# Optimization experiments

Measured on AMD Instinct MI355X. Metric: run time of the kernel, lower is better.

Reference implementation:

```python
import jax, jax.numpy as jnp
import numpy as np

N = 16384
IN_DIM = 128
OUT_DIM = 128
NUM_TYPES = 8


def setup_inputs() -> dict:
    key = jax.random.key(0)
    k1, k2, k3, k4 = jax.random.split(key, 4)
    x = jax.random.normal(k1, (N, IN_DIM), dtype=jnp.float32)
    node_types = jax.random.randint(k2, (N,), 0, NUM_TYPES, dtype=jnp.int32)
    adjacency = jax.random.uniform(k3, (N, N), dtype=jnp.float32)
    weight = jax.random.normal(k4, (NUM_TYPES, OUT_DIM, IN_DIM), dtype=jnp.float32)
    return {"x": x, "node_types": node_types, "adjacency": adjacency, "weight": weight}


def reference(x, node_types, adjacency, weight):
    # agg = A @ x : (N, in_dim)
    agg = jnp.matmul(adjacency, x)
    # Per-type projection: compute agg @ W[t].T for all types, then select
    # by node type. (N, T, out) intermediate is small (N*T*out floats).
    per_type = jnp.einsum("nd,tod->nto", agg, weight)  # (N, T, out)
    out = jnp.take_along_axis(per_type, node_types[:, None, None].astype(jnp.int32), axis=1)
    return out[:, 0, :]  # (N, out)
```

## Files before the change

### kernel.cpp

```cpp
#include <hip/hip_runtime.h>
#include <stdint.h>


#define N_NODES 16384
#define DIM     128
#define NTYPES  8
#define BM      64
#define BK      128
#define NT_K    (N_NODES / BK)

typedef float  f32x4  __attribute__((ext_vector_type(4)));
typedef __bf16 bf16x8 __attribute__((ext_vector_type(8)));

__device__ __attribute__((aligned(16))) unsigned short g_xT[DIM * N_NODES];
__device__ __attribute__((aligned(16))) unsigned short g_Wb[NTYPES * DIM * DIM];

__device__ __forceinline__ unsigned int f2b(float f) {
    unsigned int u = __float_as_uint(f);
    u += 0x7FFFu + ((u >> 16) & 1u);
    return u >> 16;
}
#define BF_LO(u) __uint_as_float((unsigned int)(u) << 16)
#define BF_HI(u) __uint_as_float((unsigned int)(u) & 0xFFFF0000u)

__device__ __forceinline__ bf16x8 cvt8(const f32x4 lo, const f32x4 hi) {
    bf16x8 r;
    r[0] = (__bf16)lo[0]; r[1] = (__bf16)lo[1]; r[2] = (__bf16)lo[2]; r[3] = (__bf16)lo[3];
    r[4] = (__bf16)hi[0]; r[5] = (__bf16)hi[1]; r[6] = (__bf16)hi[2]; r[7] = (__bf16)hi[3];
    return r;
}


__global__ void prep_all(const float* __restrict__ x, const float* __restrict__ w) {
    const int tid = threadIdx.x;
    if (blockIdx.x < 64) {
        int n = blockIdx.x * 256 + tid;
        const float* row = x + (size_t)n * DIM;
#pragma unroll
        for (int d0 = 0; d0 < DIM; d0 += 4) {
            float4 v = *(const float4*)(row + d0);
            g_xT[(d0 + 0) * N_NODES + n] = (unsigned short)f2b(v.x);
            g_xT[(d0 + 1) * N_NODES + n] = (unsigned short)f2b(v.y);
            g_xT[(d0 + 2) * N_NODES + n] = (unsigned short)f2b(v.z);
            g_xT[(d0 + 3) * N_NODES + n] = (unsigned short)f2b(v.w);
        }
    } else {
        int base = ((blockIdx.x - 64) * 256 + tid) * 16;
#pragma unroll
        for (int j = 0; j < 4; ++j) {
            float4 v = *(const float4*)(w + base + j * 4);
            ushort4 o;
            o.x = (unsigned short)f2b(v.x); o.y = (unsigned short)f2b(v.y);
            o.z = (unsigned short)f2b(v.z); o.w = (unsigned short)f2b(v.w);
            *(ushort4*)(g_Wb + base + j * 4) = o;
        }
    }
}


#define ABYTES 32768
#define XBYTES 32768

#define GLOAD16(g, l) __builtin_amdgcn_global_load_lds(                         \
    (const __attribute__((address_space(1))) unsigned int*)(g),                 \
    (__attribute__((address_space(3))) unsigned int*)(l), 16, 0, 0)

#define DMA8(Ab, Xb) do {                                                       \
    GLOAD16(gA0, (Ab) + wq);          GLOAD16(gA1, (Ab) +  8192 + wq);          \
    GLOAD16(gA2, (Ab) + 16384 + wq);  GLOAD16(gA3, (Ab) + 24576 + wq);          \
    GLOAD16(gX0, (Xb) + wq);          GLOAD16(gX1, (Xb) +  8192 + wq);          \
    GLOAD16(gX2, (Xb) + 16384 + wq);  GLOAD16(gX3, (Xb) + 24576 + wq);          \
    gA0 += BK; gA1 += BK; gA2 += BK; gA3 += BK;                                 \
    gX0 += BK; gX1 += BK; gX2 += BK; gX3 += BK;                                 \
} while (0)

#define KSUB(Ab, Xb, kc, xo) do {                                               \
    f32x4 _e = *(const f32x4*)((Ab) + aoE + (kc) * 128);                        \
    f32x4 _o = *(const f32x4*)((Ab) + aoO + (kc) * 128);                        \
    bf16x8 _a = cvt8(_e, _o);                                                   \
    bf16x8 _b0 = *(const bf16x8*)((Xb) + (xo));                                 \
    bf16x8 _b1 = *(const bf16x8*)((Xb) + (xo) + 4096);                          \
    bf16x8 _b2 = *(const bf16x8*)((Xb) + (xo) + 8192);                          \
    bf16x8 _b3 = *(const bf16x8*)((Xb) + (xo) + 12288);                         \
    acc0 = __builtin_amdgcn_mfma_f32_16x16x32_bf16(_a, _b0, acc0, 0, 0, 0);     \
    acc1 = __builtin_amdgcn_mfma_f32_16x16x32_bf16(_a, _b1, acc1, 0, 0, 0);     \
    acc2 = __builtin_amdgcn_mfma_f32_16x16x32_bf16(_a, _b2, acc2, 0, 0, 0);     \
    acc3 = __builtin_amdgcn_mfma_f32_16x16x32_bf16(_a, _b3, acc3, 0, 0, 0);     \
} while (0)

#define COMPUTE(Ab, Xb) do {        \
    KSUB(Ab, Xb, 0, xo0);           \
    KSUB(Ab, Xb, 1, xo1);           \
    KSUB(Ab, Xb, 2, xo2);           \
    KSUB(Ab, Xb, 3, xo3);           \
} while (0)

#define PHASE_I(Ac, Xc) do {                                 \
    asm volatile("s_waitcnt vmcnt(8)" ::: "memory");         \
    __builtin_amdgcn_s_barrier();                            \
    COMPUTE(Ac, Xc);                                         \
    asm volatile("s_barrier" ::: "memory");                  \
    DMA8(Ac, Xc);                                            \
} while (0)

__global__ __launch_bounds__(512, 1) void gconv_main(
    const float* __restrict__ adj,
    const int* __restrict__ types,
    float* __restrict__ out)
{
    __shared__ __align__(16) unsigned char lds[2 * (ABYTES + XBYTES)];
    unsigned char* Ab0 = lds;
    unsigned char* Ab1 = lds + ABYTES;
    unsigned char* Xb0 = lds + 2 * ABYTES;
    unsigned char* Xb1 = Xb0 + XBYTES;

    const int tid  = threadIdx.x;
    const int w    = tid >> 6;
    const int l    = tid & 63;
    const int m0   = blockIdx.x * BM;

    const int mrow = (w & 3) * 16;
    const int ncol = (w >> 2) * 64;

    f32x4 acc0 = {}, acc1 = {}, acc2 = {}, acc3 = {};

    const int arw = 2 * w + (l >> 5);
    const float* gA0 = adj + (size_t)(m0 + arw) * N_NODES
                     + (((l & 31) ^ (arw & 7)) << 2);
    const float* gA1 = gA0 + (size_t)16 * N_NODES;
    const float* gA2 = gA0 + (size_t)32 * N_NODES;
    const float* gA3 = gA0 + (size_t)48 * N_NODES;
    const int xdw = 4 * w + (l >> 4);
    const unsigned short* gX0 = g_xT + (size_t)xdw * N_NODES
                              + (((l & 15) ^ (xdw & 7)) << 3);
    const unsigned short* gX1 = gX0 + (size_t)32 * N_NODES;
    const unsigned short* gX2 = gX0 + (size_t)64 * N_NODES;
    const unsigned short* gX3 = gX0 + (size_t)96 * N_NODES;
    const int wq = w << 10;

    const int r    = mrow + (l & 15);
    const int aoE  = r * 512 + ((((l >> 4) * 2)     ^ (l & 7)) << 4);
    const int aoO  = r * 512 + ((((l >> 4) * 2 + 1) ^ (l & 7)) << 4);
    const int dd   = (ncol + (l & 15)) * 256;
    const int xo0  = dd + ((( 0 + (l >> 4)) ^ (l & 7)) << 4);
    const int xo1  = dd + ((( 4 + (l >> 4)) ^ (l & 7)) << 4);
    const int xo2  = dd + ((( 8 + (l >> 4)) ^ (l & 7)) << 4);
    const int xo3  = dd + (((12 + (l >> 4)) ^ (l & 7)) << 4);

    DMA8(Ab0, Xb0);
    DMA8(Ab1, Xb1);

    for (int i = 0; i < 63; ++i) {
        PHASE_I(Ab0, Xb0);
        PHASE_I(Ab1, Xb1);
    }
    asm volatile("s_waitcnt vmcnt(8)" ::: "memory");
    __builtin_amdgcn_s_barrier();
    COMPUTE(Ab0, Xb0);
    asm volatile("s_waitcnt vmcnt(0)" ::: "memory");
    __builtin_amdgcn_s_barrier();
    COMPUTE(Ab1, Xb1);
    __syncthreads();

    float* agg = (float*)lds;
#pragma unroll
    for (int rr = 0; rr < 4; ++rr) {
        const int gr = (mrow + (l >> 4) * 4 + rr) * 132 + ncol + (l & 15);
        agg[gr +  0] = acc0[rr];
        agg[gr + 16] = acc1[rr];
        agg[gr + 32] = acc2[rr];
        agg[gr + 48] = acc3[rr];
    }
    __syncthreads();

    const int rbase = w * 8;
    for (int rr = 0; rr < 8; ++rr) {
        const int rw = rbase + rr;
        const int nn = m0 + rw;
        const int ty = types[nn];
        const unsigned short* Wt = g_Wb + ty * (DIM * DIM);
        const int o0 = l * 2;
        const float* aggRow = agg + rw * 132;
        float s0 = 0.f, s1 = 0.f;
#pragma unroll
        for (int d0 = 0; d0 < DIM; d0 += 8) {
            float4 ga = *(const float4*)(aggRow + d0);
            float4 gb = *(const float4*)(aggRow + d0 + 4);
            uint4 wa = *(const uint4*)(Wt + o0 * DIM + d0);
            uint4 wb = *(const uint4*)(Wt + (o0 + 1) * DIM + d0);
            s0 += ga.x * BF_LO(wa.x) + ga.y * BF_HI(wa.x) + ga.z * BF_LO(wa.y) + ga.w * BF_HI(wa.y);
            s0 += gb.x * BF_LO(wa.z) + gb.y * BF_HI(wa.z) + gb.z * BF_LO(wa.w) + gb.w * BF_HI(wa.w);
            s1 += ga.x * BF_LO(wb.x) + ga.y * BF_HI(wb.x) + ga.z * BF_LO(wb.y) + ga.w * BF_HI(wb.y);
            s1 += gb.x * BF_LO(wb.z) + gb.y * BF_HI(wb.z) + gb.z * BF_LO(wb.w) + gb.w * BF_HI(wb.w);
        }
        float2 res; res.x = s0; res.y = s1;
        *(float2*)(out + (size_t)nn * DIM + o0) = res;
    }
}


extern "C" void kernel_launch(void* const* d_in, const int* in_sizes, int n_in,
                              void* d_out, int out_size, void* d_ws, size_t ws_size,
                              hipStream_t stream) {
    const float* x     = (const float*)d_in[0];
    const int*   types = (const int*)d_in[1];
    const float* adj   = (const float*)d_in[2];
    const float* wt    = (const float*)d_in[3];
    float* out = (float*)d_out;

    hipLaunchKernelGGL(prep_all, dim3(96), dim3(256), 0, stream, x, wt);
    hipLaunchKernelGGL(gconv_main, dim3(N_NODES / BM), dim3(512), 0, stream, adj, types, out);
}
```

Before: 310.4 us.

## Read bf16 x operand directly from global and triple-buffer adjacency tiles in LDS

Drops the LDS staging of the transposed bf16 x tile. Each wave now loads its B fragments straight from global memory (L2-resident) into registers, which frees LDS for a three-stage ring of adjacency buffers. The adjacency loads use a nontemporal cache-policy bit, and sched_barriers pin the issue order so that global loads overlap the MFMAs with one barrier per stage. The trade-off is that repeated per-wave global reads of x replace the shared LDS reuse, and register pressure from 16 fragment registers goes up.

```diff
diff --git a/kernel.cpp b/kernel.cpp
--- a/kernel.cpp
+++ b/kernel.cpp
@@ -59,48 +59,67 @@
 
 
 #define ABYTES 32768
-#define XBYTES 32768
-
-#define GLOAD16(g, l) __builtin_amdgcn_global_load_lds(                         \
+
+#define GLOADNT(g, l) __builtin_amdgcn_global_load_lds(                         \
     (const __attribute__((address_space(1))) unsigned int*)(g),                 \
-    (__attribute__((address_space(3))) unsigned int*)(l), 16, 0, 0)
-
-#define DMA8(Ab, Xb) do {                                                       \
-    GLOAD16(gA0, (Ab) + wq);          GLOAD16(gA1, (Ab) +  8192 + wq);          \
-    GLOAD16(gA2, (Ab) + 16384 + wq);  GLOAD16(gA3, (Ab) + 24576 + wq);          \
-    GLOAD16(gX0, (Xb) + wq);          GLOAD16(gX1, (Xb) +  8192 + wq);          \
-    GLOAD16(gX2, (Xb) + 16384 + wq);  GLOAD16(gX3, (Xb) + 24576 + wq);          \
+    (__attribute__((address_space(3))) unsigned int*)(l), 16, 0, 2)
+
+#define ISSUE_A(Ab) do {                                                        \
+    GLOADNT(gA0, (Ab) + wq);          GLOADNT(gA1, (Ab) +  8192 + wq);          \
+    GLOADNT(gA2, (Ab) + 16384 + wq);  GLOADNT(gA3, (Ab) + 24576 + wq);          \
     gA0 += BK; gA1 += BK; gA2 += BK; gA3 += BK;                                 \
-    gX0 += BK; gX1 += BK; gX2 += BK; gX3 += BK;                                 \
-} while (0)
-
-#define KSUB(Ab, Xb, kc, xo) do {                                               \
+} while (0)
+
+#define KSUB(Ab, kc, X0_, X1_, X2_, X3_) do {                                   \
     f32x4 _e = *(const f32x4*)((Ab) + aoE + (kc) * 128);                        \
     f32x4 _o = *(const f32x4*)((Ab) + aoO + (kc) * 128);                        \
     bf16x8 _a = cvt8(_e, _o);                                                   \
-    bf16x8 _b0 = *(const bf16x8*)((Xb) + (xo));                                 \
-    bf16x8 _b1 = *(const bf16x8*)((Xb) + (xo) + 4096);                          \
-    bf16x8 _b2 = *(const bf16x8*)((Xb) + (xo) + 8192);                          \
-    bf16x8 _b3 = *(const bf16x8*)((Xb) + (xo) + 12288);                         \
-    acc0 = __builtin_amdgcn_mfma_f32_16x16x32_bf16(_a, _b0, acc0, 0, 0, 0);     \
-    acc1 = __builtin_amdgcn_mfma_f32_16x16x32_bf16(_a, _b1, acc1, 0, 0, 0);     \
-    acc2 = __builtin_amdgcn_mfma_f32_16x16x32_bf16(_a, _b2, acc2, 0, 0, 0);     \
-    acc3 = __builtin_amdgcn_mfma_f32_16x16x32_bf16(_a, _b3, acc3, 0, 0, 0);     \
-} while (0)
-
-#define COMPUTE(Ab, Xb) do {        \
-    KSUB(Ab, Xb, 0, xo0);           \
-    KSUB(Ab, Xb, 1, xo1);           \
-    KSUB(Ab, Xb, 2, xo2);           \
-    KSUB(Ab, Xb, 3, xo3);           \
-} while (0)
-
-#define PHASE_I(Ac, Xc) do {                                 \
-    asm volatile("s_waitcnt vmcnt(8)" ::: "memory");         \
-    __builtin_amdgcn_s_barrier();                            \
-    COMPUTE(Ac, Xc);                                         \
-    asm volatile("s_barrier" ::: "memory");                  \
-    DMA8(Ac, Xc);                                            \
+    acc0 = __builtin_amdgcn_mfma_f32_16x16x32_bf16(_a, X0_, acc0, 0, 0, 0);     \
+    acc1 = __builtin_amdgcn_mfma_f32_16x16x32_bf16(_a, X1_, acc1, 0, 0, 0);     \
+    acc2 = __builtin_amdgcn_mfma_f32_16x16x32_bf16(_a, X2_, acc2, 0, 0, 0);     \
+    acc3 = __builtin_amdgcn_mfma_f32_16x16x32_bf16(_a, X3_, acc3, 0, 0, 0);     \
+} while (0)
+
+#define SB() __builtin_amdgcn_sched_barrier(0x10F)
+
+#define PH_I(Ac, Ai) do {                                                       \
+    asm volatile("s_waitcnt vmcnt(4)" ::: "memory");                            \
+    __builtin_amdgcn_s_barrier();                                               \
+    bf16x8 x00 = *(const bf16x8*)(bx0);      bf16x8 x01 = *(const bf16x8*)(bx1);      \
+    bf16x8 x02 = *(const bf16x8*)(bx2);      bf16x8 x03 = *(const bf16x8*)(bx3);      \
+    bf16x8 x10 = *(const bf16x8*)(bx0 + 32); bf16x8 x11 = *(const bf16x8*)(bx1 + 32); \
+    bf16x8 x12 = *(const bf16x8*)(bx2 + 32); bf16x8 x13 = *(const bf16x8*)(bx3 + 32); \
+    bf16x8 x20 = *(const bf16x8*)(bx0 + 64); bf16x8 x21 = *(const bf16x8*)(bx1 + 64); \
+    bf16x8 x22 = *(const bf16x8*)(bx2 + 64); bf16x8 x23 = *(const bf16x8*)(bx3 + 64); \
+    bf16x8 x30 = *(const bf16x8*)(bx0 + 96); bf16x8 x31 = *(const bf16x8*)(bx1 + 96); \
+    bf16x8 x32 = *(const bf16x8*)(bx2 + 96); bf16x8 x33 = *(const bf16x8*)(bx3 + 96); \
+    SB();                                                                       \
+    ISSUE_A(Ai);                                                                \
+    SB();                                                                       \
+    KSUB(Ac, 0, x00, x01, x02, x03);                                            \
+    KSUB(Ac, 1, x10, x11, x12, x13);                                            \
+    KSUB(Ac, 2, x20, x21, x22, x23);                                            \
+    KSUB(Ac, 3, x30, x31, x32, x33);                                            \
+    bx0 += BK; bx1 += BK; bx2 += BK; bx3 += BK;                                 \
+} while (0)
+
+#define PH_N(Ac, VM) do {                                                       \
+    asm volatile("s_waitcnt vmcnt(" VM ")" ::: "memory");                       \
+    __builtin_amdgcn_s_barrier();                                               \
+    bf16x8 x00 = *(const bf16x8*)(bx0);      bf16x8 x01 = *(const bf16x8*)(bx1);      \
+    bf16x8 x02 = *(const bf16x8*)(bx2);      bf16x8 x03 = *(const bf16x8*)(bx3);      \
+    bf16x8 x10 = *(const bf16x8*)(bx0 + 32); bf16x8 x11 = *(const bf16x8*)(bx1 + 32); \
+    bf16x8 x12 = *(const bf16x8*)(bx2 + 32); bf16x8 x13 = *(const bf16x8*)(bx3 + 32); \
+    bf16x8 x20 = *(const bf16x8*)(bx0 + 64); bf16x8 x21 = *(const bf16x8*)(bx1 + 64); \
+    bf16x8 x22 = *(const bf16x8*)(bx2 + 64); bf16x8 x23 = *(const bf16x8*)(bx3 + 64); \
+    bf16x8 x30 = *(const bf16x8*)(bx0 + 96); bf16x8 x31 = *(const bf16x8*)(bx1 + 96); \
+    bf16x8 x32 = *(const bf16x8*)(bx2 + 96); bf16x8 x33 = *(const bf16x8*)(bx3 + 96); \
+    SB();                                                                       \
+    KSUB(Ac, 0, x00, x01, x02, x03);                                            \
+    KSUB(Ac, 1, x10, x11, x12, x13);                                            \
+    KSUB(Ac, 2, x20, x21, x22, x23);                                            \
+    KSUB(Ac, 3, x30, x31, x32, x33);                                            \
+    bx0 += BK; bx1 += BK; bx2 += BK; bx3 += BK;                                 \
 } while (0)
 
 __global__ __launch_bounds__(512, 1) void gconv_main(
@@ -108,11 +127,10 @@
     const int* __restrict__ types,
     float* __restrict__ out)
 {
-    __shared__ __align__(16) unsigned char lds[2 * (ABYTES + XBYTES)];
+    __shared__ __align__(16) unsigned char lds[3 * ABYTES];
     unsigned char* Ab0 = lds;
     unsigned char* Ab1 = lds + ABYTES;
-    unsigned char* Xb0 = lds + 2 * ABYTES;
-    unsigned char* Xb1 = Xb0 + XBYTES;
+    unsigned char* Ab2 = lds + 2 * ABYTES;
 
     const int tid  = threadIdx.x;
     const int w    = tid >> 6;
@@ -130,36 +148,27 @@
     const float* gA1 = gA0 + (size_t)16 * N_NODES;
     const float* gA2 = gA0 + (size_t)32 * N_NODES;
     const float* gA3 = gA0 + (size_t)48 * N_NODES;
-    const int xdw = 4 * w + (l >> 4);
-    const unsigned short* gX0 = g_xT + (size_t)xdw * N_NODES
-                              + (((l & 15) ^ (xdw & 7)) << 3);
-    const unsigned short* gX1 = gX0 + (size_t)32 * N_NODES;
-    const unsigned short* gX2 = gX0 + (size_t)64 * N_NODES;
-    const unsigned short* gX3 = gX0 + (size_t)96 * N_NODES;
     const int wq = w << 10;
 
-    const int r    = mrow + (l & 15);
-    const int aoE  = r * 512 + ((((l >> 4) * 2)     ^ (l & 7)) << 4);
-    const int aoO  = r * 512 + ((((l >> 4) * 2 + 1) ^ (l & 7)) << 4);
-    const int dd   = (ncol + (l & 15)) * 256;
-    const int xo0  = dd + ((( 0 + (l >> 4)) ^ (l & 7)) << 4);
-    const int xo1  = dd + ((( 4 + (l >> 4)) ^ (l & 7)) << 4);
-    const int xo2  = dd + ((( 8 + (l >> 4)) ^ (l & 7)) << 4);
-    const int xo3  = dd + (((12 + (l >> 4)) ^ (l & 7)) << 4);
-
-    DMA8(Ab0, Xb0);
-    DMA8(Ab1, Xb1);
-
-    for (int i = 0; i < 63; ++i) {
-        PHASE_I(Ab0, Xb0);
-        PHASE_I(Ab1, Xb1);
-    }
-    asm volatile("s_waitcnt vmcnt(8)" ::: "memory");
-    __builtin_amdgcn_s_barrier();
-    COMPUTE(Ab0, Xb0);
-    asm volatile("s_waitcnt vmcnt(0)" ::: "memory");
-    __builtin_amdgcn_s_barrier();
-    COMPUTE(Ab1, Xb1);
+    const int r   = mrow + (l & 15);
+    const int aoE = r * 512 + ((((l >> 4) * 2)     ^ (l & 7)) << 4);
+    const int aoO = r * 512 + ((((l >> 4) * 2 + 1) ^ (l & 7)) << 4);
+
+    const unsigned short* bx0 = g_xT + (size_t)(ncol +  0 + (l & 15)) * N_NODES + ((l >> 4) << 3);
+    const unsigned short* bx1 = g_xT + (size_t)(ncol + 16 + (l & 15)) * N_NODES + ((l >> 4) << 3);
+    const unsigned short* bx2 = g_xT + (size_t)(ncol + 32 + (l & 15)) * N_NODES + ((l >> 4) << 3);
+    const unsigned short* bx3 = g_xT + (size_t)(ncol + 48 + (l & 15)) * N_NODES + ((l >> 4) << 3);
+
+    ISSUE_A(Ab0);
+    ISSUE_A(Ab1);
+
+    for (int i = 0; i < 42; ++i) {
+        PH_I(Ab0, Ab2);
+        PH_I(Ab1, Ab0);
+        PH_I(Ab2, Ab1);
+    }
+    PH_N(Ab0, "4");
+    PH_N(Ab1, "0");
     __syncthreads();
 
     float* agg = (float*)lds;
```

After: 608.7 us. 1.96x slower.

## Load X tiles directly into registers and give each wave private A buffers

Applied to the files above, without the earlier changes.

The main loop is restructured so each wave streams its own 16 adjacency rows into a wave-private double-buffered LDS region. The bf16 X^T fragments are loaded straight into registers with inline global_load_dwordx4, also double-buffered. This removes the workgroup barriers and the shared X staging from the K loop, so waves synchronise only through their own vmcnt waits. In exchange, waves that share the same rows now fetch the same adjacency data separately, and each wave fetches X on its own. That raises global and L2 traffic and register pressure, and relies on L2 to absorb the duplicate reads.

```diff
diff --git a/kernel.cpp b/kernel.cpp
--- a/kernel.cpp
+++ b/kernel.cpp
@@ -58,49 +58,54 @@
 }
 
 
-#define ABYTES 32768
-#define XBYTES 32768
-
 #define GLOAD16(g, l) __builtin_amdgcn_global_load_lds(                         \
     (const __attribute__((address_space(1))) unsigned int*)(g),                 \
     (__attribute__((address_space(3))) unsigned int*)(l), 16, 0, 0)
 
-#define DMA8(Ab, Xb) do {                                                       \
-    GLOAD16(gA0, (Ab) + wq);          GLOAD16(gA1, (Ab) +  8192 + wq);          \
-    GLOAD16(gA2, (Ab) + 16384 + wq);  GLOAD16(gA3, (Ab) + 24576 + wq);          \
-    GLOAD16(gX0, (Xb) + wq);          GLOAD16(gX1, (Xb) +  8192 + wq);          \
-    GLOAD16(gX2, (Xb) + 16384 + wq);  GLOAD16(gX3, (Xb) + 24576 + wq);          \
-    gA0 += BK; gA1 += BK; gA2 += BK; gA3 += BK;                                 \
-    gX0 += BK; gX1 += BK; gX2 += BK; gX3 += BK;                                 \
-} while (0)
-
-#define KSUB(Ab, Xb, kc, xo) do {                                               \
+#define XLOAD(reg, ptr, off) \
+    asm volatile("global_load_dwordx4 %0, %1, off offset:" #off : "=v"(reg) : "v"(ptr))
+
+#define ISSUE_X(P) do {                                              \
+    XLOAD(P##00, bx0,   0); XLOAD(P##01, bx1,   0);                  \
+    XLOAD(P##02, bx2,   0); XLOAD(P##03, bx3,   0);                  \
+    XLOAD(P##10, bx0,  64); XLOAD(P##11, bx1,  64);                  \
+    XLOAD(P##12, bx2,  64); XLOAD(P##13, bx3,  64);                  \
+    XLOAD(P##20, bx0, 128); XLOAD(P##21, bx1, 128);                  \
+    XLOAD(P##22, bx2, 128); XLOAD(P##23, bx3, 128);                  \
+    XLOAD(P##30, bx0, 192); XLOAD(P##31, bx1, 192);                  \
+    XLOAD(P##32, bx2, 192); XLOAD(P##33, bx3, 192);                  \
+    bx0 += BK; bx1 += BK; bx2 += BK; bx3 += BK;                      \
+} while (0)
+
+#define ISSUE_A(Abase) do {                                          \
+    GLOAD16(pA0, (Abase) + 0 * 1024);  GLOAD16(pA1, (Abase) + 1 * 1024);  \
+    GLOAD16(pA2, (Abase) + 2 * 1024);  GLOAD16(pA3, (Abase) + 3 * 1024);  \
+    GLOAD16(pA4, (Abase) + 4 * 1024);  GLOAD16(pA5, (Abase) + 5 * 1024);  \
+    GLOAD16(pA6, (Abase) + 6 * 1024);  GLOAD16(pA7, (Abase) + 7 * 1024);  \
+    pA0 += BK; pA1 += BK; pA2 += BK; pA3 += BK;                      \
+    pA4 += BK; pA5 += BK; pA6 += BK; pA7 += BK;                      \
+} while (0)
+
+#define KSUB(Ab, kc, X0_, X1_, X2_, X3_) do {                                   \
     f32x4 _e = *(const f32x4*)((Ab) + aoE + (kc) * 128);                        \
     f32x4 _o = *(const f32x4*)((Ab) + aoO + (kc) * 128);                        \
     bf16x8 _a = cvt8(_e, _o);                                                   \
-    bf16x8 _b0 = *(const bf16x8*)((Xb) + (xo));                                 \
-    bf16x8 _b1 = *(const bf16x8*)((Xb) + (xo) + 4096);                          \
-    bf16x8 _b2 = *(const bf16x8*)((Xb) + (xo) + 8192);                          \
-    bf16x8 _b3 = *(const bf16x8*)((Xb) + (xo) + 12288);                         \
-    acc0 = __builtin_amdgcn_mfma_f32_16x16x32_bf16(_a, _b0, acc0, 0, 0, 0);     \
-    acc1 = __builtin_amdgcn_mfma_f32_16x16x32_bf16(_a, _b1, acc1, 0, 0, 0);     \
-    acc2 = __builtin_amdgcn_mfma_f32_16x16x32_bf16(_a, _b2, acc2, 0, 0, 0);     \
-    acc3 = __builtin_amdgcn_mfma_f32_16x16x32_bf16(_a, _b3, acc3, 0, 0, 0);     \
-} while (0)
-
-#define COMPUTE(Ab, Xb) do {        \
-    KSUB(Ab, Xb, 0, xo0);           \
-    KSUB(Ab, Xb, 1, xo1);           \
-    KSUB(Ab, Xb, 2, xo2);           \
-    KSUB(Ab, Xb, 3, xo3);           \
-} while (0)
-
-#define PHASE_I(Ac, Xc) do {                                 \
-    asm volatile("s_waitcnt vmcnt(8)" ::: "memory");         \
-    __builtin_amdgcn_s_barrier();                            \
-    COMPUTE(Ac, Xc);                                         \
-    asm volatile("s_barrier" ::: "memory");                  \
-    DMA8(Ac, Xc);                                            \
+    acc0 = __builtin_amdgcn_mfma_f32_16x16x32_bf16(_a, X0_, acc0, 0, 0, 0);     \
+    acc1 = __builtin_amdgcn_mfma_f32_16x16x32_bf16(_a, X1_, acc1, 0, 0, 0);     \
+    acc2 = __builtin_amdgcn_mfma_f32_16x16x32_bf16(_a, X2_, acc2, 0, 0, 0);     \
+    acc3 = __builtin_amdgcn_mfma_f32_16x16x32_bf16(_a, X3_, acc3, 0, 0, 0);     \
+} while (0)
+
+#define COMPUTE(P, Ab) do {                                  \
+    KSUB(Ab, 0, P##00, P##01, P##02, P##03);                 \
+    KSUB(Ab, 1, P##10, P##11, P##12, P##13);                 \
+    KSUB(Ab, 2, P##20, P##21, P##22, P##23);                 \
+    KSUB(Ab, 3, P##30, P##31, P##32, P##33);                 \
+} while (0)
+
+#define WAITV(N) do {                                        \
+    asm volatile("s_waitcnt vmcnt(" #N ")" ::: "memory");    \
+    __builtin_amdgcn_sched_barrier(0);                       \
 } while (0)
 
 __global__ __launch_bounds__(512, 1) void gconv_main(
@@ -108,11 +113,7 @@
     const int* __restrict__ types,
     float* __restrict__ out)
 {
-    __shared__ __align__(16) unsigned char lds[2 * (ABYTES + XBYTES)];
-    unsigned char* Ab0 = lds;
-    unsigned char* Ab1 = lds + ABYTES;
-    unsigned char* Xb0 = lds + 2 * ABYTES;
-    unsigned char* Xb1 = Xb0 + XBYTES;
+    __shared__ __align__(16) unsigned char lds[8 * 16384];
 
     const int tid  = threadIdx.x;
     const int w    = tid >> 6;
@@ -122,50 +123,57 @@
     const int mrow = (w & 3) * 16;
     const int ncol = (w >> 2) * 64;
 
+    unsigned char* AbA = lds + w * 16384;
+    unsigned char* AbB = AbA + 8192;
+
     f32x4 acc0 = {}, acc1 = {}, acc2 = {}, acc3 = {};
 
-    const int arw = 2 * w + (l >> 5);
-    const float* gA0 = adj + (size_t)(m0 + arw) * N_NODES
-                     + (((l & 31) ^ (arw & 7)) << 2);
-    const float* gA1 = gA0 + (size_t)16 * N_NODES;
-    const float* gA2 = gA0 + (size_t)32 * N_NODES;
-    const float* gA3 = gA0 + (size_t)48 * N_NODES;
-    const int xdw = 4 * w + (l >> 4);
-    const unsigned short* gX0 = g_xT + (size_t)xdw * N_NODES
-                              + (((l & 15) ^ (xdw & 7)) << 3);
-    const unsigned short* gX1 = gX0 + (size_t)32 * N_NODES;
-    const unsigned short* gX2 = gX0 + (size_t)64 * N_NODES;
-    const unsigned short* gX3 = gX0 + (size_t)96 * N_NODES;
-    const int wq = w << 10;
-
-    const int r    = mrow + (l & 15);
-    const int aoE  = r * 512 + ((((l >> 4) * 2)     ^ (l & 7)) << 4);
-    const int aoO  = r * 512 + ((((l >> 4) * 2 + 1) ^ (l & 7)) << 4);
-    const int dd   = (ncol + (l & 15)) * 256;
-    const int xo0  = dd + ((( 0 + (l >> 4)) ^ (l & 7)) << 4);
-    const int xo1  = dd + ((( 4 + (l >> 4)) ^ (l & 7)) << 4);
-    const int xo2  = dd + ((( 8 + (l >> 4)) ^ (l & 7)) << 4);
-    const int xo3  = dd + (((12 + (l >> 4)) ^ (l & 7)) << 4);
-
-    DMA8(Ab0, Xb0);
-    DMA8(Ab1, Xb1);
+    const int r0 = (l >> 5);
+    const float* pA0 = adj + (size_t)(m0 + mrow +  0 + r0) * N_NODES + (((l & 31) ^ ((mrow +  0 + r0) & 7)) << 2);
+    const float* pA1 = adj + (size_t)(m0 + mrow +  2 + r0) * N_NODES + (((l & 31) ^ ((mrow +  2 + r0) & 7)) << 2);
+    const float* pA2 = adj + (size_t)(m0 + mrow +  4 + r0) * N_NODES + (((l & 31) ^ ((mrow +  4 + r0) & 7)) << 2);
+    const float* pA3 = adj + (size_t)(m0 + mrow +  6 + r0) * N_NODES + (((l & 31) ^ ((mrow +  6 + r0) & 7)) << 2);
+    const float* pA4 = adj + (size_t)(m0 + mrow +  8 + r0) * N_NODES + (((l & 31) ^ ((mrow +  8 + r0) & 7)) << 2);
+    const float* pA5 = adj + (size_t)(m0 + mrow + 10 + r0) * N_NODES + (((l & 31) ^ ((mrow + 10 + r0) & 7)) << 2);
+    const float* pA6 = adj + (size_t)(m0 + mrow + 12 + r0) * N_NODES + (((l & 31) ^ ((mrow + 12 + r0) & 7)) << 2);
+    const float* pA7 = adj + (size_t)(m0 + mrow + 14 + r0) * N_NODES + (((l & 31) ^ ((mrow + 14 + r0) & 7)) << 2);
+
+    const int h   = l >> 4;
+    const int aoE = (l & 15) * 512 + (((2 * h)     ^ (l & 7)) << 4);
+    const int aoO = (l & 15) * 512 + (((2 * h + 1) ^ (l & 7)) << 4);
+
+    const unsigned short* bx0 = g_xT + (size_t)(ncol +  0 + (l & 15)) * N_NODES + h * 8;
+    const unsigned short* bx1 = g_xT + (size_t)(ncol + 16 + (l & 15)) * N_NODES + h * 8;
+    const unsigned short* bx2 = g_xT + (size_t)(ncol + 32 + (l & 15)) * N_NODES + h * 8;
+    const unsigned short* bx3 = g_xT + (size_t)(ncol + 48 + (l & 15)) * N_NODES + h * 8;
+
+    bf16x8 p00, p01, p02, p03, p10, p11, p12, p13,
+           p20, p21, p22, p23, p30, p31, p32, p33;
+    bf16x8 q00, q01, q02, q03, q10, q11, q12, q13,
+           q20, q21, q22, q23, q30, q31, q32, q33;
+
+    ISSUE_X(p);
+    ISSUE_A(AbA);
 
     for (int i = 0; i < 63; ++i) {
-        PHASE_I(Ab0, Xb0);
-        PHASE_I(Ab1, Xb1);
-    }
-    asm volatile("s_waitcnt vmcnt(8)" ::: "memory");
-    __builtin_amdgcn_s_barrier();
-    COMPUTE(Ab0, Xb0);
-    asm volatile("s_waitcnt vmcnt(0)" ::: "memory");
-    __builtin_amdgcn_s_barrier();
-    COMPUTE(Ab1, Xb1);
+        ISSUE_X(q); ISSUE_A(AbB);
+        WAITV(24);
+        COMPUTE(p, AbA);
+        ISSUE_X(p); ISSUE_A(AbA);
+        WAITV(24);
+        COMPUTE(q, AbB);
+    }
+    ISSUE_X(q); ISSUE_A(AbB);
+    WAITV(24);
+    COMPUTE(p, AbA);
+    WAITV(0);
+    COMPUTE(q, AbB);
     __syncthreads();
 
     float* agg = (float*)lds;
 #pragma unroll
     for (int rr = 0; rr < 4; ++rr) {
-        const int gr = (mrow + (l >> 4) * 4 + rr) * 132 + ncol + (l & 15);
+        const int gr = (mrow + h * 4 + rr) * 132 + ncol + (l & 15);
         agg[gr +  0] = acc0[rr];
         agg[gr + 16] = acc1[rr];
         agg[gr + 32] = acc2[rr];
```

Measured after the change: 705.0 us. 127% more time.
